# Kernel tuning notes

Hardware: AMD Instinct MI355X
Metric: run time of the kernel (lower is better)

The kernel has to match this reference:

```python
import jax, jax.numpy as jnp
from jax import lax
import numpy as np

DIM = 48
HEADS = 2
HIDDEN = 96  # int(dim * 2.0)
EPS_LN = 1e-5
EPS_NORM = 1e-12


def _ln(x, w, b):
    # WithBias LayerNorm over channel dim (dim=1 in NCHW == last dim in b,(hw),c)
    mu = jnp.mean(x, axis=1, keepdims=True)
    var = jnp.var(x, axis=1, keepdims=True)
    return (x - mu) / jnp.sqrt(var + EPS_LN) * w[None, :, None, None] + b[None, :, None, None]


def _conv1x1(x, w, b):
    # w: [O, C, 1, 1]
    return jnp.einsum('bchw,oc->bohw', x, w[:, :, 0, 0]) + b[None, :, None, None]


def _dwconv3(x, w, b):
    # w: [C, 1, 3, 3], groups=C
    y = lax.conv_general_dilated(x, w, (1, 1), 'SAME',
                                 feature_group_count=x.shape[1],
                                 dimension_numbers=('NCHW', 'OIHW', 'NCHW'))
    return y + b[None, :, None, None]


def _l2norm(x):
    n = jnp.sqrt(jnp.sum(x * x, axis=-1, keepdims=True))
    return x / jnp.maximum(n, EPS_NORM)


def setup_inputs() -> dict:
    key = jax.random.key(0)
    ks = jax.random.split(key, 12)
    s = 0.02
    inp = {
        'x': jax.random.normal(ks[0], (2, DIM, 64, 64), jnp.float32),
        'norm1_w': jnp.ones((DIM,), jnp.float32),
        'norm1_b': jnp.zeros((DIM,), jnp.float32),
        'qkv_w': jax.random.normal(ks[1], (DIM * 3, DIM, 1, 1), jnp.float32) * s,
        'qkv_b': jnp.zeros((DIM * 3,), jnp.float32),
        'qkvdw_w': jax.random.normal(ks[2], (DIM * 3, 1, 3, 3), jnp.float32) * s,
        'qkvdw_b': jnp.zeros((DIM * 3,), jnp.float32),
        'temperature': jnp.ones((HEADS, 1, 1), jnp.float32),
        'proj_w': jax.random.normal(ks[3], (DIM, DIM, 1, 1), jnp.float32) * s,
        'proj_b': jnp.zeros((DIM,), jnp.float32),
        'norm2_w': jnp.ones((DIM,), jnp.float32),
        'norm2_b': jnp.zeros((DIM,), jnp.float32),
        'fi_w': jax.random.normal(ks[4], (HIDDEN * 2, DIM, 1, 1), jnp.float32) * s,
        'fi_b': jnp.zeros((HIDDEN * 2,), jnp.float32),
        'fdw_w': jax.random.normal(ks[5], (HIDDEN * 2, 1, 3, 3), jnp.float32) * s,
        'fdw_b': jnp.zeros((HIDDEN * 2,), jnp.float32),
        'fo_w': jax.random.normal(ks[6], (DIM, HIDDEN, 1, 1), jnp.float32) * s,
        'fo_b': jnp.zeros((DIM,), jnp.float32),
    }
    return inp


def _block(x, norm1_w, norm1_b, qkv_w, qkv_b, qkvdw_w, qkvdw_b, temperature,
           proj_w, proj_b, norm2_w, norm2_b, fi_w, fi_b, fdw_w, fdw_b, fo_w, fo_b):
    b, c, h, w = x.shape
    n = h * w
    chead = c // HEADS
    # --- attention branch ---
    xn = _ln(x, norm1_w, norm1_b)
    qkv = _dwconv3(_conv1x1(xn, qkv_w, qkv_b), qkvdw_w, qkvdw_b)
    q, k, v = jnp.split(qkv, 3, axis=1)
    def to_heads(t):  # [b, heads*chead, h, w] -> [b, heads, n, chead]
        return t.reshape(b, HEADS, chead, n).transpose(0, 1, 3, 2)
    q, k, v = to_heads(q), to_heads(k), to_heads(v)
    q = _l2norm(q)
    k = _l2norm(k)
    attn = jnp.einsum('bhnc,bhmc->bhnm', q, k) * temperature[None]
    attn = jax.nn.softmax(attn, axis=-1)
    out = jnp.einsum('bhnm,bhmc->bhnc', attn, v)
    out = out.transpose(0, 1, 3, 2).reshape(b, c, h, w)
    x = x + _conv1x1(out, proj_w, proj_b)
    # --- ffn branch ---
    xn = _ln(x, norm2_w, norm2_b)
    y = _dwconv3(_conv1x1(xn, fi_w, fi_b), fdw_w, fdw_b)
    y1, y2 = jnp.split(y, 2, axis=1)
    y = jax.nn.gelu(y1, approximate=False) * y2
    x = x + _conv1x1(y, fo_w, fo_b)
    return x


def reference(x, norm1_w, norm1_b, qkv_w, qkv_b, qkvdw_w, qkvdw_b, temperature,
              proj_w, proj_b, norm2_w, norm2_b, fi_w, fi_b, fdw_w, fdw_b, fo_w, fo_b):
    return _block(x, norm1_w, norm1_b, qkv_w, qkv_b, qkvdw_w, qkvdw_b, temperature,
                  proj_w, proj_b, norm2_w, norm2_b, fi_w, fi_b, fdw_w, fdw_b, fo_w, fo_b)
```

## Files before the change

### kernel.cpp

```cpp
#include <hip/hip_runtime.h>
#include <hip/hip_bf16.h>
#include <math.h>

#define NPIX 4096
#define DIMC 48
#define NB 2
#define SPLIT 4

typedef __attribute__((ext_vector_type(8))) short short8;
typedef __attribute__((ext_vector_type(4))) short short4s;
typedef __attribute__((ext_vector_type(4))) float floatx4;

static __device__ inline short f2bf(float f) {
    union { float f; unsigned u; } v; v.f = f;
    unsigned r = (v.u + 0x7FFFu + ((v.u >> 16) & 1u)) >> 16;
    return (short)r;
}
static __device__ inline float bf2f(short s) {
    union { unsigned u; float f; } v;
    v.u = ((unsigned)(unsigned short)s) << 16;
    return v.f;
}
static __device__ inline unsigned pk2(float a, float b) {
    __hip_bfloat162 pk = __float22bfloat162_rn(make_float2(a, b));
    return *(unsigned*)&pk;
}

__global__ void k_prepw(const float* __restrict__ qkvw, const float* __restrict__ fiw,
                        const float* __restrict__ fow, const float* __restrict__ projw,
                        short* __restrict__ qkvwbf, short* __restrict__ fiwbf,
                        short* __restrict__ fowbf, short* __restrict__ projwbf) {
    int idx = blockIdx.x * 256 + threadIdx.x;
    if (idx < 144 * 64) {
        int o = idx >> 6, c = idx & 63;
        qkvwbf[idx] = (c < 48) ? f2bf(qkvw[o * 48 + c]) : (short)0;
        return;
    }
    idx -= 144 * 64;
    if (idx < 192 * 64) {
        int o = idx >> 6, c = idx & 63;
        fiwbf[idx] = (c < 48) ? f2bf(fiw[o * 48 + c]) : (short)0;
        return;
    }
    idx -= 192 * 64;
    if (idx < 48 * 96) {
        fowbf[idx] = f2bf(fow[idx]);
        return;
    }
    idx -= 48 * 96;
    if (idx < 48 * 64) {
        int o = idx >> 6, c = idx & 63;
        projwbf[idx] = (c < 48) ? f2bf(projw[o * 48 + c]) : (short)0;
    }
}

__global__ __launch_bounds__(256) void k_ln_conv_mfma(
    const float* __restrict__ xin, const float* __restrict__ lw, const float* __restrict__ lb,
    const short* __restrict__ wbf, const float* __restrict__ cb,
    short* __restrict__ outbf, int OC)
{
    int px0 = blockIdx.x * 32;
    int b = blockIdx.y;
    int t = threadIdx.x;
    int w = t >> 6, lane = t & 63, l15 = lane & 15, quad = lane >> 4;

    __shared__ float psum[8][32], psq[8][32];
    __shared__ float muS[32], rsS[32];
    __shared__ short xnbf[32][72];

    int px = t & 31, g = t >> 5;
    *(unsigned*)&xnbf[px][48 + g * 2] = 0u;

    float v[6];
    float s = 0.f, sq = 0.f;
#pragma unroll
    for (int i = 0; i < 6; i++) {
        v[i] = xin[((size_t)b * 48 + g * 6 + i) * (size_t)NPIX + px0 + px];
        s += v[i]; sq += v[i] * v[i];
    }
    psum[g][px] = s; psq[g][px] = sq;
    __syncthreads();
    if (t < 32) {
        float ss = 0.f, qq = 0.f;
#pragma unroll
        for (int i = 0; i < 8; i++) { ss += psum[i][t]; qq += psq[i][t]; }
        float mu = ss * (1.f / 48.f);
        float var = qq * (1.f / 48.f) - mu * mu;
        muS[t] = mu; rsS[t] = rsqrtf(var + 1e-5f);
    }
    __syncthreads();
    {
        float mu = muS[px], rs = rsS[px];
#pragma unroll
        for (int i = 0; i < 6; i++) {
            int c = g * 6 + i;
            xnbf[px][c] = f2bf((v[i] - mu) * rs * lw[c] + lb[c]);
        }
    }
    __syncthreads();
    floatx4 zf = {0.f, 0.f, 0.f, 0.f};
    int oct = OC >> 4;
    int njobs = 2 * oct;
    for (int job = w; job < njobs; job += 4) {
        int pt = job / oct, ot = job % oct;
        short8 a0 = *(const short8*)&xnbf[pt * 16 + l15][quad * 8];
        short8 a1 = *(const short8*)&xnbf[pt * 16 + l15][32 + quad * 8];
        const short* wb = wbf + (ot * 16 + l15) * 64;
        short8 b0 = *(const short8*)(wb + quad * 8);
        short8 b1 = *(const short8*)(wb + 32 + quad * 8);
        floatx4 c = __builtin_amdgcn_mfma_f32_16x16x32_bf16(a0, b0, zf, 0, 0, 0);
        c = __builtin_amdgcn_mfma_f32_16x16x32_bf16(a1, b1, c, 0, 0, 0);
        int oc = ot * 16 + l15;
        float bi = cb[oc];
        short4s st;
#pragma unroll
        for (int r = 0; r < 4; r++) st[r] = f2bf(c[r] + bi);
        *(short4s*)(outbf + ((size_t)b * OC + oc) * (size_t)NPIX + px0 + pt * 16 + quad * 4) = st;
    }
}

__global__ __launch_bounds__(256) void k_dw3heads(
    const short* __restrict__ qkv_pre, const float* __restrict__ dww,
    const float* __restrict__ dwb, const float* __restrict__ temp,
    short* __restrict__ Qbf, short* __restrict__ Kbf, short* __restrict__ Vbf)
{
    int px0 = blockIdx.x * 16;
    int y = blockIdx.y, b = blockIdx.z;
    int t = threadIdx.x;
    int wx0 = px0 - 8; if (wx0 < 0) wx0 = 0; if (wx0 > 32) wx0 = 32;
    int xoff = px0 - wx0;

    __shared__ short stage[3][144][40];
    __shared__ float q2[16][148];

    for (int seg = t; seg < 3 * 144 * 4; seg += 256) {
        int q = seg & 3, idx = seg >> 2;
        int c = idx % 144, r = idx / 144;
        int yy = y + r - 1;
        short8 ld = {};
        if ((unsigned)yy < 64u)
            ld = *(const short8*)(qkv_pre + (size_t)(b * 144 + c) * NPIX + yy * 64 + wx0 + q * 8);
        *(short8*)&stage[r][c][q * 8] = ld;
    }
    __syncthreads();
    int px = t & 15, g = t >> 4;
    {
        int sbase = xoff + px;
        for (int i = 0; i < 9; i++) {
            int c = g * 9 + i;
            const float* wp = dww + c * 9;
            float acc = dwb[c];
#pragma unroll
            for (int dy = 0; dy < 3; dy++) {
#pragma unroll
                for (int dx = -1; dx <= 1; dx++) {
                    int si = sbase + dx;
                    if ((unsigned)si < 32u)
                        acc += bf2f(stage[dy][c][si]) * wp[dy * 3 + dx + 1];
                }
            }
            q2[px][c] = acc;
        }
    }
    __syncthreads();
    if (t < 32) {
        int hpx = t & 15, h = t >> 4;
        int n = y * 64 + px0 + hpx;
        int bh = b * 2 + h;
        float q[24], k[24], vv[24]; float sqs = 0.f, sks = 0.f;
#pragma unroll
        for (int c = 0; c < 24; c++) {
            q[c] = q2[hpx][h * 24 + c];       sqs += q[c] * q[c];
            k[c] = q2[hpx][48 + h * 24 + c];  sks += k[c] * k[c];
            vv[c] = q2[hpx][96 + h * 24 + c];
        }
        float rq = temp[h] / fmaxf(sqrtf(sqs), 1e-12f);
        float rk = 1.f / fmaxf(sqrtf(sks), 1e-12f);
        short qs[32], ks[32];
#pragma unroll
        for (int c = 0; c < 24; c++) { qs[c] = f2bf(q[c] * rq); ks[c] = f2bf(k[c] * rk); }
#pragma unroll
        for (int c = 24; c < 32; c++) { qs[c] = 0; ks[c] = 0; }
        size_t ro = ((size_t)bh * NPIX + n) * 32;
#pragma unroll
        for (int i = 0; i < 4; i++) {
            short8 a, bb;
#pragma unroll
            for (int j = 0; j < 8; j++) { a[j] = qs[i * 8 + j]; bb[j] = ks[i * 8 + j]; }
            *(short8*)(Qbf + ro + i * 8) = a;
            *(short8*)(Kbf + ro + i * 8) = bb;
        }
        int r5 = n & 31;
        int pos = (r5 < 16) ? ((r5 >> 2) * 8 + (r5 & 3))
                            : (((r5 & 15) >> 2) * 8 + (r5 & 3) + 4);
        int vcol = (n & ~31) + pos;
#pragma unroll
        for (int c = 0; c < 24; c++)
            Vbf[((size_t)bh * 32 + c) * NPIX + vcol] = f2bf(vv[c]);
#pragma unroll
        for (int c = 24; c < 32; c++)
            Vbf[((size_t)bh * 32 + c) * NPIX + vcol] = 0;
    }
}

__global__ __launch_bounds__(256) void k_attn_mfma(const short* __restrict__ Qbf,
                                                   const short* __restrict__ Kbf,
                                                   const short* __restrict__ Vbf,
                                                   float* __restrict__ Opart,
                                                   float* __restrict__ lpart) {
    int qt = blockIdx.x, s = blockIdx.y, bh = blockIdx.z;
    int t = threadIdx.x;
    int w = t >> 6, lane = t & 63, l15 = lane & 15, quad = lane >> 4;

    __shared__ short tileK[2][64][40];
    __shared__ short tileV[2][32][72];

    int qrow0 = qt * 64 + w * 16;
    short8 bq = *(const short8*)(Qbf + ((size_t)bh * NPIX + qrow0 + l15) * 32 + quad * 8);

    int krow = t >> 2, kseg = t & 3;
    int vch = t >> 3, vseg = t & 7;
    const short* srcK = Kbf + ((size_t)bh * NPIX + krow) * 32 + kseg * 8;
    const short* srcV = Vbf + ((size_t)(bh * 32 + vch)) * NPIX + vseg * 8;

    int key0 = s * (NPIX / SPLIT);
    *(short8*)&tileK[0][krow][kseg * 8] = *(const short8*)(srcK + (size_t)key0 * 32);
    *(short8*)&tileV[0][vch][vseg * 8]  = *(const short8*)(srcV + key0);

    floatx4 zf = {0.f, 0.f, 0.f, 0.f};
    floatx4 o0 = zf, o1 = zf;
    float ls = 0.f;

    const int NKT = (NPIX / SPLIT) / 64;
    for (int kt = 0; kt < NKT; kt++) {
        __syncthreads();
        int cur = kt & 1;
        short8 ldK = {}, ldV = {};
        if (kt < NKT - 1) {
            int kabs = key0 + (kt + 1) * 64;
            ldK = *(const short8*)(srcK + (size_t)kabs * 32);
            ldV = *(const short8*)(srcV + kabs);
        }
        short8 ka0 = *(const short8*)&tileK[cur][l15][quad * 8];
        short8 ka1 = *(const short8*)&tileK[cur][16 + l15][quad * 8];
        short8 ka2 = *(const short8*)&tileK[cur][32 + l15][quad * 8];
        short8 ka3 = *(const short8*)&tileK[cur][48 + l15][quad * 8];
        floatx4 s0 = __builtin_amdgcn_mfma_f32_16x16x32_bf16(ka0, bq, zf, 0, 0, 0);
        floatx4 s1 = __builtin_amdgcn_mfma_f32_16x16x32_bf16(ka1, bq, zf, 0, 0, 0);
        floatx4 s2 = __builtin_amdgcn_mfma_f32_16x16x32_bf16(ka2, bq, zf, 0, 0, 0);
        floatx4 s3 = __builtin_amdgcn_mfma_f32_16x16x32_bf16(ka3, bq, zf, 0, 0, 0);
        float e0[4], e1[4], e2[4], e3[4];
#pragma unroll
        for (int r = 0; r < 4; r++) {
            e0[r] = __expf(s0[r]); e1[r] = __expf(s1[r]);
            e2[r] = __expf(s2[r]); e3[r] = __expf(s3[r]);
            ls += (e0[r] + e1[r]) + (e2[r] + e3[r]);
        }
        short8 p01, p23;
        {
            unsigned* u01 = (unsigned*)&p01;
            unsigned* u23 = (unsigned*)&p23;
            u01[0] = pk2(e0[0], e0[1]); u01[1] = pk2(e0[2], e0[3]);
            u01[2] = pk2(e1[0], e1[1]); u01[3] = pk2(e1[2], e1[3]);
            u23[0] = pk2(e2[0], e2[1]); u23[1] = pk2(e2[2], e2[3]);
            u23[2] = pk2(e3[0], e3[1]); u23[3] = pk2(e3[2], e3[3]);
        }
        short8 va00 = *(const short8*)&tileV[cur][l15][quad * 8];
        short8 va01 = *(const short8*)&tileV[cur][l15][32 + quad * 8];
        short8 va10 = *(const short8*)&tileV[cur][16 + l15][quad * 8];
        short8 va11 = *(const short8*)&tileV[cur][16 + l15][32 + quad * 8];
        o0 = __builtin_amdgcn_mfma_f32_16x16x32_bf16(va00, p01, o0, 0, 0, 0);
        o0 = __builtin_amdgcn_mfma_f32_16x16x32_bf16(va01, p23, o0, 0, 0, 0);
        o1 = __builtin_amdgcn_mfma_f32_16x16x32_bf16(va10, p01, o1, 0, 0, 0);
        o1 = __builtin_amdgcn_mfma_f32_16x16x32_bf16(va11, p23, o1, 0, 0, 0);
        if (kt < NKT - 1) {
            *(short8*)&tileK[1 - cur][krow][kseg * 8] = ldK;
            *(short8*)&tileV[1 - cur][vch][vseg * 8]  = ldV;
        }
    }
    ls += __shfl_xor(ls, 16, 64);
    ls += __shfl_xor(ls, 32, 64);
    int n = qrow0 + l15;
    size_t base2 = (size_t)(bh * SPLIT + s) * 32;
#pragma unroll
    for (int r = 0; r < 4; r++) {
        Opart[(base2 + quad * 4 + r) * NPIX + n] = o0[r];
        Opart[(base2 + 16 + quad * 4 + r) * NPIX + n] = o1[r];
    }
    if (quad == 0) lpart[((size_t)(bh * SPLIT + s)) * NPIX + n] = ls;
}

__global__ __launch_bounds__(256) void k_projlnfi(
    const float* __restrict__ x, const float* __restrict__ Opart,
    const float* __restrict__ lpart, const short* __restrict__ projwbf,
    const float* __restrict__ projb,
    const float* __restrict__ n2w, const float* __restrict__ n2b,
    const short* __restrict__ fiwbf, const float* __restrict__ fib,
    float* __restrict__ x1, short* __restrict__ fp_pre)
{
    int px0 = blockIdx.x * 32;
    int b = blockIdx.y;
    int t = threadIdx.x;
    int w = t >> 6, lane = t & 63, l15 = lane & 15, quad = lane >> 4;

    __shared__ __align__(16) short Ash[32][72];
    __shared__ float rlsh[2][32];
    __shared__ float x1sh[32][53];
    __shared__ float psum[8][32], psq[8][32];
    __shared__ float muS[32], rsS[32];
    __shared__ short xnbf[32][72];

    if (t < 64) {
        int h = t >> 5, px = t & 31;
        float l = 0.f;
#pragma unroll
        for (int s = 0; s < SPLIT; s++)
            l += lpart[((size_t)((b * 2 + h) * SPLIT + s)) * NPIX + px0 + px];
        rlsh[h][px] = 1.f / l;
    }
    {
        int px = t & 31, j = t >> 5;
        *(unsigned*)&Ash[px][48 + j * 2] = 0u;
        *(unsigned*)&xnbf[px][48 + j * 2] = 0u;
    }
    __syncthreads();
#pragma unroll
    for (int pi = 0; pi < 6; pi++) {
        int idx = pi * 256 + t;
        int px = idx & 31, c = idx >> 5;
        int h = c / 24, ch = c % 24;
        float acc = 0.f;
#pragma unroll
        for (int s = 0; s < SPLIT; s++)
            acc += Opart[(((size_t)((b * 2 + h) * SPLIT + s)) * 32 + ch) * NPIX + px0 + px];
        Ash[px][c] = f2bf(acc * rlsh[h][px]);
    }
    __syncthreads();
    floatx4 zf = {0.f, 0.f, 0.f, 0.f};
    for (int job = w; job < 6; job += 4) {
        int pt = job / 3, ot = job % 3;
        short8 a0 = *(const short8*)&Ash[pt * 16 + l15][quad * 8];
        short8 a1 = *(const short8*)&Ash[pt * 16 + l15][32 + quad * 8];
        const short* wb = projwbf + (ot * 16 + l15) * 64;
        short8 b0 = *(const short8*)(wb + quad * 8);
        short8 b1 = *(const short8*)(wb + 32 + quad * 8);
        floatx4 c = __builtin_amdgcn_mfma_f32_16x16x32_bf16(a0, b0, zf, 0, 0, 0);
        c = __builtin_amdgcn_mfma_f32_16x16x32_bf16(a1, b1, c, 0, 0, 0);
        int oc = ot * 16 + l15;
        float bi = projb[oc];
#pragma unroll
        for (int r = 0; r < 4; r++) {
            int px = pt * 16 + quad * 4 + r;
            size_t idx = ((size_t)b * 48 + oc) * NPIX + px0 + px;
            float val = x[idx] + c[r] + bi;
            x1[idx] = val;
            x1sh[px][oc] = val;
        }
    }
    __syncthreads();
    int px = t & 31, g = t >> 5;
    float v[6];
    float s = 0.f, sq = 0.f;
#pragma unroll
    for (int i = 0; i < 6; i++) {
        v[i] = x1sh[px][g * 6 + i];
        s += v[i]; sq += v[i] * v[i];
    }
    psum[g][px] = s; psq[g][px] = sq;
    __syncthreads();
    if (t < 32) {
        float ss = 0.f, qq = 0.f;
#pragma unroll
        for (int i = 0; i < 8; i++) { ss += psum[i][t]; qq += psq[i][t]; }
        float mu = ss * (1.f / 48.f);
        float var = qq * (1.f / 48.f) - mu * mu;
        muS[t] = mu; rsS[t] = rsqrtf(var + 1e-5f);
    }
    __syncthreads();
    {
        float mu = muS[px], rs = rsS[px];
#pragma unroll
        for (int i = 0; i < 6; i++) {
            int c = g * 6 + i;
            xnbf[px][c] = f2bf((v[i] - mu) * rs * n2w[c] + n2b[c]);
        }
    }
    __syncthreads();
    for (int job = w; job < 24; job += 4) {
        int pt = job / 12, ot = job % 12;
        short8 a0 = *(const short8*)&xnbf[pt * 16 + l15][quad * 8];
        short8 a1 = *(const short8*)&xnbf[pt * 16 + l15][32 + quad * 8];
        const short* wb = fiwbf + (ot * 16 + l15) * 64;
        short8 b0 = *(const short8*)(wb + quad * 8);
        short8 b1 = *(const short8*)(wb + 32 + quad * 8);
        floatx4 c = __builtin_amdgcn_mfma_f32_16x16x32_bf16(a0, b0, zf, 0, 0, 0);
        c = __builtin_amdgcn_mfma_f32_16x16x32_bf16(a1, b1, c, 0, 0, 0);
        int oc = ot * 16 + l15;
        float bi = fib[oc];
        short4s st;
#pragma unroll
        for (int r = 0; r < 4; r++) st[r] = f2bf(c[r] + bi);
        *(short4s*)(fp_pre + ((size_t)b * 192 + oc) * (size_t)NPIX + px0 + pt * 16 + quad * 4) = st;
    }
}

__global__ __launch_bounds__(256) void k_dwgatefo(
    const short* __restrict__ fp_pre, const float* __restrict__ fdww,
    const float* __restrict__ fdwb, const short* __restrict__ fowbf,
    const float* __restrict__ fob, const float* __restrict__ x1,
    float* __restrict__ out)
{
    int px0 = blockIdx.x * 16;
    int y = blockIdx.y, b = blockIdx.z;
    int t = threadIdx.x;
    int w = t >> 6, lane = t & 63, l15 = lane & 15, quad = lane >> 4;
    int wx0 = px0 - 8; if (wx0 < 0) wx0 = 0; if (wx0 > 32) wx0 = 32;
    int xoff = px0 - wx0;

    __shared__ short stage[3][192][40];
    __shared__ short yv[16][104];

    for (int seg = t; seg < 3 * 192 * 4; seg += 256) {
        int q = seg & 3, idx = seg >> 2;
        int c = idx % 192, r = idx / 192;
        int yy = y + r - 1;
        short8 ld = {};
        if ((unsigned)yy < 64u)
            ld = *(const short8*)(fp_pre + (size_t)(b * 192 + c) * NPIX + yy * 64 + wx0 + q * 8);
        *(short8*)&stage[r][c][q * 8] = ld;
    }
    __syncthreads();
    int px = t & 15, g = t >> 4;
    {
        int sbase = xoff + px;
        for (int i = 0; i < 6; i++) {
            int c = g * 6 + i;
            const float* wp  = fdww + c * 9;
            const float* wp2 = fdww + (c + 96) * 9;
            float a  = fdwb[c];
            float g2 = fdwb[c + 96];
#pragma unroll
            for (int dy = 0; dy < 3; dy++) {
#pragma unroll
                for (int dx = -1; dx <= 1; dx++) {
                    int si = sbase + dx;
                    if ((unsigned)si < 32u) {
                        a  += bf2f(stage[dy][c][si])      * wp[dy * 3 + dx + 1];
                        g2 += bf2f(stage[dy][c + 96][si]) * wp2[dy * 3 + dx + 1];
                    }
                }
            }
            float ge = 0.5f * a * (1.f + erff(a * 0.70710678118654752f));
            yv[px][c] = f2bf(ge * g2);
        }
    }
    __syncthreads();
    if (w < 3) {
        floatx4 c = {0.f, 0.f, 0.f, 0.f};
#pragma unroll
        for (int k = 0; k < 3; k++) {
            short8 a = *(const short8*)&yv[l15][k * 32 + quad * 8];
            short8 bb = *(const short8*)(fowbf + (w * 16 + l15) * 96 + k * 32 + quad * 8);
            c = __builtin_amdgcn_mfma_f32_16x16x32_bf16(a, bb, c, 0, 0, 0);
        }
        int oc = w * 16 + l15;
        float bi = fob[oc];
#pragma unroll
        for (int r = 0; r < 4; r++) {
            int n = y * 64 + px0 + quad * 4 + r;
            size_t idx = ((size_t)b * 48 + oc) * NPIX + n;
            out[idx] = x1[idx] + c[r] + bi;
        }
    }
}

extern "C" void kernel_launch(void* const* d_in, const int* in_sizes, int n_in,
                              void* d_out, int out_size, void* d_ws, size_t ws_size,
                              hipStream_t stream) {
    const float* x       = (const float*)d_in[0];
    const float* n1w     = (const float*)d_in[1];
    const float* n1b     = (const float*)d_in[2];
    const float* qkv_w   = (const float*)d_in[3];
    const float* qkv_b   = (const float*)d_in[4];
    const float* qkvdw_w = (const float*)d_in[5];
    const float* qkvdw_b = (const float*)d_in[6];
    const float* temp    = (const float*)d_in[7];
    const float* proj_w  = (const float*)d_in[8];
    const float* proj_b  = (const float*)d_in[9];
    const float* n2w     = (const float*)d_in[10];
    const float* n2b     = (const float*)d_in[11];
    const float* fi_w    = (const float*)d_in[12];
    const float* fi_b    = (const float*)d_in[13];
    const float* fdw_w   = (const float*)d_in[14];
    const float* fdw_b   = (const float*)d_in[15];
    const float* fo_w    = (const float*)d_in[16];
    const float* fo_b    = (const float*)d_in[17];

    float* ws = (float*)d_ws;
    short* qkv_pre = (short*)ws;
    short* fp_pre  = (short*)(ws + 589824);
    short* Qbf     = (short*)(ws + 1376256);
    short* Kbf     = (short*)(ws + 1638400);
    short* Vbf     = (short*)(ws + 1900544);
    float* Opart   = ws + 2162688;
    float* lpart   = ws + 4259840;
    float* x1      = ws + 4325376;
    short* qkvwbf  = (short*)(ws + 4718592);
    short* fiwbf   = qkvwbf + 9216;
    short* fowbf   = fiwbf + 12288;
    short* projwbf = fowbf + 4608;

    {
        int total = 144 * 64 + 192 * 64 + 48 * 96 + 48 * 64;
        k_prepw<<<(total + 255) / 256, 256, 0, stream>>>(qkv_w, fi_w, fo_w, proj_w,
                                                         qkvwbf, fiwbf, fowbf, projwbf);
    }
    {
        dim3 g(128, NB);
        k_ln_conv_mfma<<<g, 256, 0, stream>>>(x, n1w, n1b, qkvwbf, qkv_b, qkv_pre, 144);
    }
    {
        dim3 g(4, 64, NB);
        k_dw3heads<<<g, 256, 0, stream>>>(qkv_pre, qkvdw_w, qkvdw_b, temp, Qbf, Kbf, Vbf);
    }
    {
        dim3 g(64, SPLIT, 4);
        k_attn_mfma<<<g, 256, 0, stream>>>(Qbf, Kbf, Vbf, Opart, lpart);
    }
    {
        dim3 g(128, NB);
        k_projlnfi<<<g, 256, 0, stream>>>(x, Opart, lpart, projwbf, proj_b,
                                          n2w, n2b, fiwbf, fi_b, x1, fp_pre);
    }
    {
        dim3 g(4, 64, NB);
        k_dwgatefo<<<g, 256, 0, stream>>>(fp_pre, fdw_w, fdw_b, fowbf, fo_b, x1,
                                          (float*)d_out);
    }
}
```

Baseline: 149.6 us.

## Fuse pipeline into three kernels with halo recompute and in-block attention split-K combine

```diff
diff --git a/kernel.cpp b/kernel.cpp
--- a/kernel.cpp
+++ b/kernel.cpp
@@ -3,9 +3,7 @@
 #include <math.h>
 
 #define NPIX 4096
-#define DIMC 48
 #define NB 2
-#define SPLIT 4
 
 typedef __attribute__((ext_vector_type(8))) short short8;
 typedef __attribute__((ext_vector_type(4))) short short4s;
@@ -50,188 +48,182 @@
     idx -= 48 * 96;
     if (idx < 48 * 64) {
         int o = idx >> 6, c = idx & 63;
-        projwbf[idx] = (c < 48) ? f2bf(projw[o * 48 + c]) : (short)0;
-    }
-}
-
-__global__ __launch_bounds__(256) void k_ln_conv_mfma(
-    const float* __restrict__ xin, const float* __restrict__ lw, const float* __restrict__ lb,
-    const short* __restrict__ wbf, const float* __restrict__ cb,
-    short* __restrict__ outbf, int OC)
+        int h = c >> 5, cc = c & 31;
+        projwbf[idx] = (cc < 24) ? f2bf(projw[o * 48 + h * 24 + cc]) : (short)0;
+    }
+}
+
+__global__ __launch_bounds__(256) void k_qkv_fused(
+    const float* __restrict__ xin, const float* __restrict__ n1w, const float* __restrict__ n1b,
+    const short* __restrict__ qkvwbf, const float* __restrict__ qkvb,
+    const float* __restrict__ dww, const float* __restrict__ dwb,
+    const float* __restrict__ temp,
+    short* __restrict__ Qbf, short* __restrict__ Kbf, short* __restrict__ Vbf)
 {
-    int px0 = blockIdx.x * 32;
-    int b = blockIdx.y;
+    int px0 = blockIdx.x * 16;
+    int y = blockIdx.y, b = blockIdx.z;
     int t = threadIdx.x;
     int w = t >> 6, lane = t & 63, l15 = lane & 15, quad = lane >> 4;
 
-    __shared__ float psum[8][32], psq[8][32];
-    __shared__ float muS[32], rsS[32];
-    __shared__ short xnbf[32][72];
-
-    int px = t & 31, g = t >> 5;
-    *(unsigned*)&xnbf[px][48 + g * 2] = 0u;
-
-    float v[6];
-    float s = 0.f, sq = 0.f;
-#pragma unroll
-    for (int i = 0; i < 6; i++) {
-        v[i] = xin[((size_t)b * 48 + g * 6 + i) * (size_t)NPIX + px0 + px];
-        s += v[i]; sq += v[i] * v[i];
-    }
-    psum[g][px] = s; psq[g][px] = sq;
-    __syncthreads();
-    if (t < 32) {
-        float ss = 0.f, qq = 0.f;
-#pragma unroll
-        for (int i = 0; i < 8; i++) { ss += psum[i][t]; qq += psq[i][t]; }
+    __shared__ __align__(16) short xn[64][72];
+    __shared__ short qkv[64][148];
+    __shared__ float q2[16][148];
+    __shared__ float red[4][64], redq[4][64];
+    __shared__ float muS[64], rsS[64];
+    __shared__ float dwwS[1296], dwbS[144];
+    __shared__ short vmask[64];
+
+    for (int u = t; u < 1296; u += 256) dwwS[u] = dww[u];
+    if (t < 144) dwbS[t] = dwb[t];
+
+    int pp = t & 63, cg = t >> 6;
+    int rr = pp / 18, ix = pp - rr * 18;
+    int yy = y + rr - 1, xpx = px0 - 1 + ix;
+    bool pv = (pp < 54) && ((unsigned)yy < 64u) && ((unsigned)xpx < 64u);
+    if (cg == 0) vmask[pp] = pv ? (short)1 : (short)0;
+
+    float v[12]; float s = 0.f, sq = 0.f;
+    if (pv) {
+        size_t pbase = (size_t)(yy * 64 + xpx);
+#pragma unroll
+        for (int j = 0; j < 12; j++) {
+            float vv = xin[((size_t)b * 48 + cg * 12 + j) * NPIX + pbase];
+            v[j] = vv; s += vv; sq += vv * vv;
+        }
+    } else {
+#pragma unroll
+        for (int j = 0; j < 12; j++) v[j] = 0.f;
+    }
+    red[cg][pp] = s; redq[cg][pp] = sq;
+    __syncthreads();
+    if (t < 64) {
+        float ss = red[0][t] + red[1][t] + red[2][t] + red[3][t];
+        float qq = redq[0][t] + redq[1][t] + redq[2][t] + redq[3][t];
         float mu = ss * (1.f / 48.f);
         float var = qq * (1.f / 48.f) - mu * mu;
         muS[t] = mu; rsS[t] = rsqrtf(var + 1e-5f);
     }
     __syncthreads();
     {
-        float mu = muS[px], rs = rsS[px];
-#pragma unroll
-        for (int i = 0; i < 6; i++) {
-            int c = g * 6 + i;
-            xnbf[px][c] = f2bf((v[i] - mu) * rs * lw[c] + lb[c]);
-        }
+        float mu = muS[pp], rs = rsS[pp];
+#pragma unroll
+        for (int j = 0; j < 12; j++) {
+            int c = cg * 12 + j;
+            xn[pp][c] = f2bf((v[j] - mu) * rs * n1w[c] + n1b[c]);
+        }
+        short8 z8 = {};
+        if (cg == 0) *(short8*)&xn[pp][48] = z8;
+        else if (cg == 1) *(short8*)&xn[pp][56] = z8;
     }
     __syncthreads();
     floatx4 zf = {0.f, 0.f, 0.f, 0.f};
-    int oct = OC >> 4;
-    int njobs = 2 * oct;
-    for (int job = w; job < njobs; job += 4) {
-        int pt = job / oct, ot = job % oct;
-        short8 a0 = *(const short8*)&xnbf[pt * 16 + l15][quad * 8];
-        short8 a1 = *(const short8*)&xnbf[pt * 16 + l15][32 + quad * 8];
-        const short* wb = wbf + (ot * 16 + l15) * 64;
+    for (int job = w; job < 36; job += 4) {
+        int pt = job / 9, ot = job % 9;
+        short8 a0 = *(const short8*)&xn[pt * 16 + l15][quad * 8];
+        short8 a1 = *(const short8*)&xn[pt * 16 + l15][32 + quad * 8];
+        const short* wb = qkvwbf + (ot * 16 + l15) * 64;
         short8 b0 = *(const short8*)(wb + quad * 8);
         short8 b1 = *(const short8*)(wb + 32 + quad * 8);
         floatx4 c = __builtin_amdgcn_mfma_f32_16x16x32_bf16(a0, b0, zf, 0, 0, 0);
         c = __builtin_amdgcn_mfma_f32_16x16x32_bf16(a1, b1, c, 0, 0, 0);
         int oc = ot * 16 + l15;
-        float bi = cb[oc];
-        short4s st;
-#pragma unroll
-        for (int r = 0; r < 4; r++) st[r] = f2bf(c[r] + bi);
-        *(short4s*)(outbf + ((size_t)b * OC + oc) * (size_t)NPIX + px0 + pt * 16 + quad * 4) = st;
-    }
-}
-
-__global__ __launch_bounds__(256) void k_dw3heads(
-    const short* __restrict__ qkv_pre, const float* __restrict__ dww,
-    const float* __restrict__ dwb, const float* __restrict__ temp,
-    short* __restrict__ Qbf, short* __restrict__ Kbf, short* __restrict__ Vbf)
+        float bi = qkvb[oc];
+#pragma unroll
+        for (int r = 0; r < 4; r++) {
+            int opp = pt * 16 + quad * 4 + r;
+            qkv[opp][oc] = vmask[opp] ? f2bf(c[r] + bi) : (short)0;
+        }
+    }
+    __syncthreads();
+    {
+        int i = t & 15, g = t >> 4;
+        for (int cc = 0; cc < 9; cc++) {
+            int c = g * 9 + cc;
+            const float* wp = dwwS + c * 9;
+            float acc = dwbS[c];
+#pragma unroll
+            for (int dy = 0; dy < 3; dy++)
+#pragma unroll
+                for (int dx = 0; dx < 3; dx++)
+                    acc += bf2f(qkv[dy * 18 + i + dx][c]) * wp[dy * 3 + dx];
+            q2[i][c] = acc;
+        }
+    }
+    __syncthreads();
+    if (t < 128) {
+        int i = t & 15, h = (t >> 4) & 1, sel = t >> 5;
+        int n = y * 64 + px0 + i;
+        int bh = b * 2 + h;
+        if (sel < 2) {
+            float vv2[24]; float ss = 0.f;
+            int base = sel * 48 + h * 24;
+#pragma unroll
+            for (int c = 0; c < 24; c++) { vv2[c] = q2[i][base + c]; ss += vv2[c] * vv2[c]; }
+            float sc = ((sel == 0) ? temp[h] : 1.f) / fmaxf(sqrtf(ss), 1e-12f);
+            short qs[32];
+#pragma unroll
+            for (int c = 0; c < 24; c++) qs[c] = f2bf(vv2[c] * sc);
+#pragma unroll
+            for (int c = 24; c < 32; c++) qs[c] = 0;
+            short* dst = ((sel == 0) ? Qbf : Kbf) + ((size_t)bh * NPIX + n) * 32;
+#pragma unroll
+            for (int i8 = 0; i8 < 4; i8++) {
+                short8 st;
+#pragma unroll
+                for (int j = 0; j < 8; j++) st[j] = qs[i8 * 8 + j];
+                *(short8*)(dst + i8 * 8) = st;
+            }
+        } else {
+            int half = sel - 2;
+            int r5 = n & 31;
+            int pos = (r5 < 16) ? ((r5 >> 2) * 8 + (r5 & 3))
+                                : (((r5 & 15) >> 2) * 8 + (r5 & 3) + 4);
+            int vcol = (n & ~31) + pos;
+#pragma unroll
+            for (int cc = 0; cc < 12; cc++) {
+                int c = half * 12 + cc;
+                Vbf[((size_t)bh * 32 + c) * NPIX + vcol] = f2bf(q2[i][96 + h * 24 + c]);
+            }
+            if (half == 1) {
+#pragma unroll
+                for (int c = 24; c < 32; c++)
+                    Vbf[((size_t)bh * 32 + c) * NPIX + vcol] = 0;
+            }
+        }
+    }
+}
+
+__global__ __launch_bounds__(1024) void k_attn_mfma2(
+    const short* __restrict__ Qbf, const short* __restrict__ Kbf,
+    const short* __restrict__ Vbf, short* __restrict__ O)
 {
-    int px0 = blockIdx.x * 16;
-    int y = blockIdx.y, b = blockIdx.z;
+    int qt = blockIdx.x, bh = blockIdx.y;
     int t = threadIdx.x;
-    int wx0 = px0 - 8; if (wx0 < 0) wx0 = 0; if (wx0 > 32) wx0 = 32;
-    int xoff = px0 - wx0;
-
-    __shared__ short stage[3][144][40];
-    __shared__ float q2[16][148];
-
-    for (int seg = t; seg < 3 * 144 * 4; seg += 256) {
-        int q = seg & 3, idx = seg >> 2;
-        int c = idx % 144, r = idx / 144;
-        int yy = y + r - 1;
-        short8 ld = {};
-        if ((unsigned)yy < 64u)
-            ld = *(const short8*)(qkv_pre + (size_t)(b * 144 + c) * NPIX + yy * 64 + wx0 + q * 8);
-        *(short8*)&stage[r][c][q * 8] = ld;
-    }
-    __syncthreads();
-    int px = t & 15, g = t >> 4;
-    {
-        int sbase = xoff + px;
-        for (int i = 0; i < 9; i++) {
-            int c = g * 9 + i;
-            const float* wp = dww + c * 9;
-            float acc = dwb[c];
-#pragma unroll
-            for (int dy = 0; dy < 3; dy++) {
-#pragma unroll
-                for (int dx = -1; dx <= 1; dx++) {
-                    int si = sbase + dx;
-                    if ((unsigned)si < 32u)
-                        acc += bf2f(stage[dy][c][si]) * wp[dy * 3 + dx + 1];
-                }
-            }
-            q2[px][c] = acc;
-        }
-    }
-    __syncthreads();
-    if (t < 32) {
-        int hpx = t & 15, h = t >> 4;
-        int n = y * 64 + px0 + hpx;
-        int bh = b * 2 + h;
-        float q[24], k[24], vv[24]; float sqs = 0.f, sks = 0.f;
-#pragma unroll
-        for (int c = 0; c < 24; c++) {
-            q[c] = q2[hpx][h * 24 + c];       sqs += q[c] * q[c];
-            k[c] = q2[hpx][48 + h * 24 + c];  sks += k[c] * k[c];
-            vv[c] = q2[hpx][96 + h * 24 + c];
-        }
-        float rq = temp[h] / fmaxf(sqrtf(sqs), 1e-12f);
-        float rk = 1.f / fmaxf(sqrtf(sks), 1e-12f);
-        short qs[32], ks[32];
-#pragma unroll
-        for (int c = 0; c < 24; c++) { qs[c] = f2bf(q[c] * rq); ks[c] = f2bf(k[c] * rk); }
-#pragma unroll
-        for (int c = 24; c < 32; c++) { qs[c] = 0; ks[c] = 0; }
-        size_t ro = ((size_t)bh * NPIX + n) * 32;
-#pragma unroll
-        for (int i = 0; i < 4; i++) {
-            short8 a, bb;
-#pragma unroll
-            for (int j = 0; j < 8; j++) { a[j] = qs[i * 8 + j]; bb[j] = ks[i * 8 + j]; }
-            *(short8*)(Qbf + ro + i * 8) = a;
-            *(short8*)(Kbf + ro + i * 8) = bb;
-        }
-        int r5 = n & 31;
-        int pos = (r5 < 16) ? ((r5 >> 2) * 8 + (r5 & 3))
-                            : (((r5 & 15) >> 2) * 8 + (r5 & 3) + 4);
-        int vcol = (n & ~31) + pos;
-#pragma unroll
-        for (int c = 0; c < 24; c++)
-            Vbf[((size_t)bh * 32 + c) * NPIX + vcol] = f2bf(vv[c]);
-#pragma unroll
-        for (int c = 24; c < 32; c++)
-            Vbf[((size_t)bh * 32 + c) * NPIX + vcol] = 0;
-    }
-}
-
-__global__ __launch_bounds__(256) void k_attn_mfma(const short* __restrict__ Qbf,
-                                                   const short* __restrict__ Kbf,
-                                                   const short* __restrict__ Vbf,
-                                                   float* __restrict__ Opart,
-                                                   float* __restrict__ lpart) {
-    int qt = blockIdx.x, s = blockIdx.y, bh = blockIdx.z;
-    int t = threadIdx.x;
-    int w = t >> 6, lane = t & 63, l15 = lane & 15, quad = lane >> 4;
-
-    __shared__ short tileK[2][64][40];
-    __shared__ short tileV[2][32][72];
-
-    int qrow0 = qt * 64 + w * 16;
+    int tg = t & 255, g = t >> 8;
+    int wloc = (t >> 6) & 3, lane = t & 63, l15 = lane & 15, quad = lane >> 4;
+
+    __shared__ __align__(16) short tileK[4][2][64][40];
+    __shared__ __align__(16) short tileV[4][2][32][72];
+    __shared__ float Ocomb[4][64][33];
+    __shared__ float Lcomb[4][64];
+
+    int qrow0 = qt * 64 + wloc * 16;
     short8 bq = *(const short8*)(Qbf + ((size_t)bh * NPIX + qrow0 + l15) * 32 + quad * 8);
 
-    int krow = t >> 2, kseg = t & 3;
-    int vch = t >> 3, vseg = t & 7;
+    int krow = tg >> 2, kseg = tg & 3;
+    int vch = tg >> 3, vseg = tg & 7;
     const short* srcK = Kbf + ((size_t)bh * NPIX + krow) * 32 + kseg * 8;
     const short* srcV = Vbf + ((size_t)(bh * 32 + vch)) * NPIX + vseg * 8;
 
-    int key0 = s * (NPIX / SPLIT);
-    *(short8*)&tileK[0][krow][kseg * 8] = *(const short8*)(srcK + (size_t)key0 * 32);
-    *(short8*)&tileV[0][vch][vseg * 8]  = *(const short8*)(srcV + key0);
+    int key0 = g * 1024;
+    *(short8*)&tileK[g][0][krow][kseg * 8] = *(const short8*)(srcK + (size_t)key0 * 32);
+    *(short8*)&tileV[g][0][vch][vseg * 8]  = *(const short8*)(srcV + key0);
 
     floatx4 zf = {0.f, 0.f, 0.f, 0.f};
     floatx4 o0 = zf, o1 = zf;
     float ls = 0.f;
 
-    const int NKT = (NPIX / SPLIT) / 64;
+    const int NKT = 16;
     for (int kt = 0; kt < NKT; kt++) {
         __syncthreads();
         int cur = kt & 1;
@@ -241,10 +233,10 @@
             ldK = *(const short8*)(srcK + (size_t)kabs * 32);
             ldV = *(const short8*)(srcV + kabs);
         }
-        short8 ka0 = *(const short8*)&tileK[cur][l15][quad * 8];
-        short8 ka1 = *(const short8*)&tileK[cur][16 + l15][quad * 8];
-        short8 ka2 = *(const short8*)&tileK[cur][32 + l15][quad * 8];
-        short8 ka3 = *(const short8*)&tileK[cur][48 + l15][quad * 8];
+        short8 ka0 = *(const short8*)&tileK[g][cur][l15][quad * 8];
+        short8 ka1 = *(const short8*)&tileK[g][cur][16 + l15][quad * 8];
+        short8 ka2 = *(const short8*)&tileK[g][cur][32 + l15][quad * 8];
+        short8 ka3 = *(const short8*)&tileK[g][cur][48 + l15][quad * 8];
         floatx4 s0 = __builtin_amdgcn_mfma_f32_16x16x32_bf16(ka0, bq, zf, 0, 0, 0);
         floatx4 s1 = __builtin_amdgcn_mfma_f32_16x16x32_bf16(ka1, bq, zf, 0, 0, 0);
         floatx4 s2 = __builtin_amdgcn_mfma_f32_16x16x32_bf16(ka2, bq, zf, 0, 0, 0);
@@ -265,82 +257,86 @@
             u23[0] = pk2(e2[0], e2[1]); u23[1] = pk2(e2[2], e2[3]);
             u23[2] = pk2(e3[0], e3[1]); u23[3] = pk2(e3[2], e3[3]);
         }
-        short8 va00 = *(const short8*)&tileV[cur][l15][quad * 8];
-        short8 va01 = *(const short8*)&tileV[cur][l15][32 + quad * 8];
-        short8 va10 = *(const short8*)&tileV[cur][16 + l15][quad * 8];
-        short8 va11 = *(const short8*)&tileV[cur][16 + l15][32 + quad * 8];
+        short8 va00 = *(const short8*)&tileV[g][cur][l15][quad * 8];
+        short8 va01 = *(const short8*)&tileV[g][cur][l15][32 + quad * 8];
+        short8 va10 = *(const short8*)&tileV[g][cur][16 + l15][quad * 8];
+        short8 va11 = *(const short8*)&tileV[g][cur][16 + l15][32 + quad * 8];
         o0 = __builtin_amdgcn_mfma_f32_16x16x32_bf16(va00, p01, o0, 0, 0, 0);
         o0 = __builtin_amdgcn_mfma_f32_16x16x32_bf16(va01, p23, o0, 0, 0, 0);
         o1 = __builtin_amdgcn_mfma_f32_16x16x32_bf16(va10, p01, o1, 0, 0, 0);
         o1 = __builtin_amdgcn_mfma_f32_16x16x32_bf16(va11, p23, o1, 0, 0, 0);
         if (kt < NKT - 1) {
-            *(short8*)&tileK[1 - cur][krow][kseg * 8] = ldK;
-            *(short8*)&tileV[1 - cur][vch][vseg * 8]  = ldV;
+            *(short8*)&tileK[g][1 - cur][krow][kseg * 8] = ldK;
+            *(short8*)&tileV[g][1 - cur][vch][vseg * 8]  = ldV;
         }
     }
     ls += __shfl_xor(ls, 16, 64);
     ls += __shfl_xor(ls, 32, 64);
-    int n = qrow0 + l15;
-    size_t base2 = (size_t)(bh * SPLIT + s) * 32;
+    int qi = wloc * 16 + l15;
 #pragma unroll
     for (int r = 0; r < 4; r++) {
-        Opart[(base2 + quad * 4 + r) * NPIX + n] = o0[r];
-        Opart[(base2 + 16 + quad * 4 + r) * NPIX + n] = o1[r];
-    }
-    if (quad == 0) lpart[((size_t)(bh * SPLIT + s)) * NPIX + n] = ls;
-}
-
-__global__ __launch_bounds__(256) void k_projlnfi(
-    const float* __restrict__ x, const float* __restrict__ Opart,
-    const float* __restrict__ lpart, const short* __restrict__ projwbf,
-    const float* __restrict__ projb,
+        Ocomb[g][qi][quad * 4 + r]      = o0[r];
+        Ocomb[g][qi][16 + quad * 4 + r] = o1[r];
+    }
+    if (quad == 0) Lcomb[g][qi] = ls;
+    __syncthreads();
+    {
+        int qq = t >> 4, cp = t & 15;
+        float l4 = Lcomb[0][qq] + Lcomb[1][qq] + Lcomb[2][qq] + Lcomb[3][qq];
+        float inv = 1.f / l4;
+        float sa = (Ocomb[0][qq][2 * cp] + Ocomb[1][qq][2 * cp] +
+                    Ocomb[2][qq][2 * cp] + Ocomb[3][qq][2 * cp]) * inv;
+        float sb = (Ocomb[0][qq][2 * cp + 1] + Ocomb[1][qq][2 * cp + 1] +
+                    Ocomb[2][qq][2 * cp + 1] + Ocomb[3][qq][2 * cp + 1]) * inv;
+        int b = bh >> 1, h = bh & 1;
+        int n = qt * 64 + qq;
+        *(unsigned*)(O + ((size_t)b * NPIX + n) * 64 + h * 32 + 2 * cp) = pk2(sa, sb);
+    }
+}
+
+__global__ __launch_bounds__(256) void k_tail_fused(
+    const float* __restrict__ xin, const short* __restrict__ O,
+    const short* __restrict__ projwbf, const float* __restrict__ projb,
     const float* __restrict__ n2w, const float* __restrict__ n2b,
     const short* __restrict__ fiwbf, const float* __restrict__ fib,
-    float* __restrict__ x1, short* __restrict__ fp_pre)
+    const float* __restrict__ fdww, const float* __restrict__ fdwb,
+    const short* __restrict__ fowbf, const float* __restrict__ fob,
+    float* __restrict__ out)
 {
-    int px0 = blockIdx.x * 32;
-    int b = blockIdx.y;
+    int px0 = blockIdx.x * 16;
+    int y = blockIdx.y, b = blockIdx.z;
     int t = threadIdx.x;
     int w = t >> 6, lane = t & 63, l15 = lane & 15, quad = lane >> 4;
 
-    __shared__ __align__(16) short Ash[32][72];
-    __shared__ float rlsh[2][32];
-    __shared__ float x1sh[32][53];
-    __shared__ float psum[8][32], psq[8][32];
-    __shared__ float muS[32], rsS[32];
-    __shared__ short xnbf[32][72];
-
+    __shared__ float x1s[64][53];
+    __shared__ __align__(16) short xn2[64][72];
+    __shared__ short ypre[56][196];
+    __shared__ __align__(16) short yv[16][104];
+    __shared__ float red[4][64], redq[4][64];
+    __shared__ float muS[64], rsS[64];
+    __shared__ float fdwwS[1728], fdwbS[192];
+    __shared__ short vmask[64];
+    __shared__ int nidx[64];
+
+    for (int u = t; u < 1728; u += 256) fdwwS[u] = fdww[u];
+    if (t < 192) fdwbS[t] = fdwb[t];
     if (t < 64) {
-        int h = t >> 5, px = t & 31;
-        float l = 0.f;
-#pragma unroll
-        for (int s = 0; s < SPLIT; s++)
-            l += lpart[((size_t)((b * 2 + h) * SPLIT + s)) * NPIX + px0 + px];
-        rlsh[h][px] = 1.f / l;
-    }
-    {
-        int px = t & 31, j = t >> 5;
-        *(unsigned*)&Ash[px][48 + j * 2] = 0u;
-        *(unsigned*)&xnbf[px][48 + j * 2] = 0u;
-    }
-    __syncthreads();
-#pragma unroll
-    for (int pi = 0; pi < 6; pi++) {
-        int idx = pi * 256 + t;
-        int px = idx & 31, c = idx >> 5;
-        int h = c / 24, ch = c % 24;
-        float acc = 0.f;
-#pragma unroll
-        for (int s = 0; s < SPLIT; s++)
-            acc += Opart[(((size_t)((b * 2 + h) * SPLIT + s)) * 32 + ch) * NPIX + px0 + px];
-        Ash[px][c] = f2bf(acc * rlsh[h][px]);
-    }
-    __syncthreads();
+        int rr = t / 18, ix = t - rr * 18;
+        int yy = y + rr - 1, xpx = px0 - 1 + ix;
+        bool pv = (t < 54) && ((unsigned)yy < 64u) && ((unsigned)xpx < 64u);
+        vmask[t] = pv ? (short)1 : (short)0;
+        int n = yy * 64 + xpx;
+        n = n < 0 ? 0 : (n > 4095 ? 4095 : n);
+        nidx[t] = n;
+    }
+    __syncthreads();
+
     floatx4 zf = {0.f, 0.f, 0.f, 0.f};
-    for (int job = w; job < 6; job += 4) {
+    for (int job = w; job < 12; job += 4) {
         int pt = job / 3, ot = job % 3;
-        short8 a0 = *(const short8*)&Ash[pt * 16 + l15][quad * 8];
-        short8 a1 = *(const short8*)&Ash[pt * 16 + l15][32 + quad * 8];
+        const short* oa = O + ((size_t)b * NPIX + nidx[pt * 16 + l15]) * 64;
+        short8 a0 = *(const short8*)(oa + quad * 8);
+        short8 a1 = *(const short8*)(oa + 32 + quad * 8);
         const short* wb = projwbf + (ot * 16 + l15) * 64;
         short8 b0 = *(const short8*)(wb + quad * 8);
         short8 b1 = *(const short8*)(wb + 32 + quad * 8);
@@ -350,46 +346,44 @@
         float bi = projb[oc];
 #pragma unroll
         for (int r = 0; r < 4; r++) {
-            int px = pt * 16 + quad * 4 + r;
-            size_t idx = ((size_t)b * 48 + oc) * NPIX + px0 + px;
-            float val = x[idx] + c[r] + bi;
-            x1[idx] = val;
-            x1sh[px][oc] = val;
-        }
-    }
-    __syncthreads();
-    int px = t & 31, g = t >> 5;
-    float v[6];
-    float s = 0.f, sq = 0.f;
-#pragma unroll
-    for (int i = 0; i < 6; i++) {
-        v[i] = x1sh[px][g * 6 + i];
-        s += v[i]; sq += v[i] * v[i];
-    }
-    psum[g][px] = s; psq[g][px] = sq;
-    __syncthreads();
-    if (t < 32) {
-        float ss = 0.f, qq = 0.f;
-#pragma unroll
-        for (int i = 0; i < 8; i++) { ss += psum[i][t]; qq += psq[i][t]; }
-        float mu = ss * (1.f / 48.f);
-        float var = qq * (1.f / 48.f) - mu * mu;
-        muS[t] = mu; rsS[t] = rsqrtf(var + 1e-5f);
-    }
-    __syncthreads();
-    {
-        float mu = muS[px], rs = rsS[px];
-#pragma unroll
-        for (int i = 0; i < 6; i++) {
-            int c = g * 6 + i;
-            xnbf[px][c] = f2bf((v[i] - mu) * rs * n2w[c] + n2b[c]);
-        }
-    }
-    __syncthreads();
-    for (int job = w; job < 24; job += 4) {
+            int opp = pt * 16 + quad * 4 + r;
+            x1s[opp][oc] = xin[((size_t)b * 48 + oc) * NPIX + nidx[opp]] + c[r] + bi;
+        }
+    }
+    __syncthreads();
+    int pp = t & 63, cg = t >> 6;
+    {
+        float v[12]; float s = 0.f, sq = 0.f;
+#pragma unroll
+        for (int j = 0; j < 12; j++) {
+            float vv = x1s[pp][cg * 12 + j];
+            v[j] = vv; s += vv; sq += vv * vv;
+        }
+        red[cg][pp] = s; redq[cg][pp] = sq;
+        __syncthreads();
+        if (t < 64) {
+            float ss = red[0][t] + red[1][t] + red[2][t] + red[3][t];
+            float qq = redq[0][t] + redq[1][t] + redq[2][t] + redq[3][t];
+            float mu = ss * (1.f / 48.f);
+            float var = qq * (1.f / 48.f) - mu * mu;
+            muS[t] = mu; rsS[t] = rsqrtf(var + 1e-5f);
+        }
+        __syncthreads();
+        float mu = muS[pp], rs = rsS[pp];
+#pragma unroll
+        for (int j = 0; j < 12; j++) {
+            int c = cg * 12 + j;
+            xn2[pp][c] = f2bf((v[j] - mu) * rs * n2w[c] + n2b[c]);
+        }
+        short8 z8 = {};
+        if (cg == 0) *(short8*)&xn2[pp][48] = z8;
+        else if (cg == 1) *(short8*)&xn2[pp][56] = z8;
+    }
+    __syncthreads();
+    for (int job = w; job < 48; job += 4) {
         int pt = job / 12, ot = job % 12;
-        short8 a0 = *(const short8*)&xnbf[pt * 16 + l15][quad * 8];
-        short8 a1 = *(const short8*)&xnbf[pt * 16 + l15][32 + quad * 8];
+        short8 a0 = *(const short8*)&xn2[pt * 16 + l15][quad * 8];
+        short8 a1 = *(const short8*)&xn2[pt * 16 + l15][32 + quad * 8];
         const short* wb = fiwbf + (ot * 16 + l15) * 64;
         short8 b0 = *(const short8*)(wb + quad * 8);
         short8 b1 = *(const short8*)(wb + 32 + quad * 8);
@@ -397,69 +391,40 @@
         c = __builtin_amdgcn_mfma_f32_16x16x32_bf16(a1, b1, c, 0, 0, 0);
         int oc = ot * 16 + l15;
         float bi = fib[oc];
-        short4s st;
-#pragma unroll
-        for (int r = 0; r < 4; r++) st[r] = f2bf(c[r] + bi);
-        *(short4s*)(fp_pre + ((size_t)b * 192 + oc) * (size_t)NPIX + px0 + pt * 16 + quad * 4) = st;
-    }
-}
-
-__global__ __launch_bounds__(256) void k_dwgatefo(
-    const short* __restrict__ fp_pre, const float* __restrict__ fdww,
-    const float* __restrict__ fdwb, const short* __restrict__ fowbf,
-    const float* __restrict__ fob, const float* __restrict__ x1,
-    float* __restrict__ out)
-{
-    int px0 = blockIdx.x * 16;
-    int y = blockIdx.y, b = blockIdx.z;
-    int t = threadIdx.x;
-    int w = t >> 6, lane = t & 63, l15 = lane & 15, quad = lane >> 4;
-    int wx0 = px0 - 8; if (wx0 < 0) wx0 = 0; if (wx0 > 32) wx0 = 32;
-    int xoff = px0 - wx0;
-
-    __shared__ short stage[3][192][40];
-    __shared__ short yv[16][104];
-
-    for (int seg = t; seg < 3 * 192 * 4; seg += 256) {
-        int q = seg & 3, idx = seg >> 2;
-        int c = idx % 192, r = idx / 192;
-        int yy = y + r - 1;
-        short8 ld = {};
-        if ((unsigned)yy < 64u)
-            ld = *(const short8*)(fp_pre + (size_t)(b * 192 + c) * NPIX + yy * 64 + wx0 + q * 8);
-        *(short8*)&stage[r][c][q * 8] = ld;
-    }
-    __syncthreads();
-    int px = t & 15, g = t >> 4;
-    {
-        int sbase = xoff + px;
-        for (int i = 0; i < 6; i++) {
-            int c = g * 6 + i;
-            const float* wp  = fdww + c * 9;
-            const float* wp2 = fdww + (c + 96) * 9;
-            float a  = fdwb[c];
-            float g2 = fdwb[c + 96];
-#pragma unroll
-            for (int dy = 0; dy < 3; dy++) {
-#pragma unroll
-                for (int dx = -1; dx <= 1; dx++) {
-                    int si = sbase + dx;
-                    if ((unsigned)si < 32u) {
-                        a  += bf2f(stage[dy][c][si])      * wp[dy * 3 + dx + 1];
-                        g2 += bf2f(stage[dy][c + 96][si]) * wp2[dy * 3 + dx + 1];
-                    }
+#pragma unroll
+        for (int r = 0; r < 4; r++) {
+            int opp = pt * 16 + quad * 4 + r;
+            if (opp < 56) ypre[opp][oc] = vmask[opp] ? f2bf(c[r] + bi) : (short)0;
+        }
+    }
+    __syncthreads();
+    {
+        int i = t & 15, gg = t >> 4;
+        for (int cc = 0; cc < 6; cc++) {
+            int c = gg * 6 + cc;
+            const float* wp  = fdwwS + c * 9;
+            const float* wp2 = fdwwS + (c + 96) * 9;
+            float a = fdwbS[c], g2v = fdwbS[c + 96];
+#pragma unroll
+            for (int dy = 0; dy < 3; dy++)
+#pragma unroll
+                for (int dx = 0; dx < 3; dx++) {
+                    int ppi = dy * 18 + i + dx;
+                    a   += bf2f(ypre[ppi][c])      * wp[dy * 3 + dx];
+                    g2v += bf2f(ypre[ppi][c + 96]) * wp2[dy * 3 + dx];
                 }
-            }
             float ge = 0.5f * a * (1.f + erff(a * 0.70710678118654752f));
-            yv[px][c] = f2bf(ge * g2);
-        }
+            yv[i][c] = f2bf(ge * g2v);
+        }
+        short8 z8 = {};
+        if (gg == 0) *(short8*)&yv[i][96] = z8;
     }
     __syncthreads();
     if (w < 3) {
-        floatx4 c = {0.f, 0.f, 0.f, 0.f};
+        floatx4 c = zf;
 #pragma unroll
         for (int k = 0; k < 3; k++) {
-            short8 a = *(const short8*)&yv[l15][k * 32 + quad * 8];
+            short8 a  = *(const short8*)&yv[l15][k * 32 + quad * 8];
             short8 bb = *(const short8*)(fowbf + (w * 16 + l15) * 96 + k * 32 + quad * 8);
             c = __builtin_amdgcn_mfma_f32_16x16x32_bf16(a, bb, c, 0, 0, 0);
         }
@@ -467,9 +432,9 @@
         float bi = fob[oc];
 #pragma unroll
         for (int r = 0; r < 4; r++) {
-            int n = y * 64 + px0 + quad * 4 + r;
-            size_t idx = ((size_t)b * 48 + oc) * NPIX + n;
-            out[idx] = x1[idx] + c[r] + bi;
+            int i = quad * 4 + r;
+            size_t idx = ((size_t)b * 48 + oc) * NPIX + y * 64 + px0 + i;
+            out[idx] = x1s[19 + i][oc] + c[r] + bi;
         }
     }
 }
@@ -496,16 +461,12 @@
     const float* fo_w    = (const float*)d_in[16];
     const float* fo_b    = (const float*)d_in[17];
 
-    float* ws = (float*)d_ws;
-    short* qkv_pre = (short*)ws;
-    short* fp_pre  = (short*)(ws + 589824);
-    short* Qbf     = (short*)(ws + 1376256);
-    short* Kbf     = (short*)(ws + 1638400);
-    short* Vbf     = (short*)(ws + 1900544);
-    float* Opart   = ws + 2162688;
-    float* lpart   = ws + 4259840;
-    float* x1      = ws + 4325376;
-    short* qkvwbf  = (short*)(ws + 4718592);
+    short* sws = (short*)d_ws;
+    short* Qbf     = sws;
+    short* Kbf     = Qbf + 524288;
+    short* Vbf     = Kbf + 524288;
+    short* Obuf    = Vbf + 524288;
+    short* qkvwbf  = Obuf + 524288;
     short* fiwbf   = qkvwbf + 9216;
     short* fowbf   = fiwbf + 12288;
     short* projwbf = fowbf + 4608;
@@ -516,25 +477,18 @@
                                                          qkvwbf, fiwbf, fowbf, projwbf);
     }
     {
-        dim3 g(128, NB);
-        k_ln_conv_mfma<<<g, 256, 0, stream>>>(x, n1w, n1b, qkvwbf, qkv_b, qkv_pre, 144);
-    }
-    {
         dim3 g(4, 64, NB);
-        k_dw3heads<<<g, 256, 0, stream>>>(qkv_pre, qkvdw_w, qkvdw_b, temp, Qbf, Kbf, Vbf);
-    }
-    {
-        dim3 g(64, SPLIT, 4);
-        k_attn_mfma<<<g, 256, 0, stream>>>(Qbf, Kbf, Vbf, Opart, lpart);
-    }
-    {
-        dim3 g(128, NB);
-        k_projlnfi<<<g, 256, 0, stream>>>(x, Opart, lpart, projwbf, proj_b,
-                                          n2w, n2b, fiwbf, fi_b, x1, fp_pre);
+        k_qkv_fused<<<g, 256, 0, stream>>>(x, n1w, n1b, qkvwbf, qkv_b,
+                                           qkvdw_w, qkvdw_b, temp, Qbf, Kbf, Vbf);
+    }
+    {
+        dim3 g(64, 4);
+        k_attn_mfma2<<<g, 1024, 0, stream>>>(Qbf, Kbf, Vbf, Obuf);
     }
     {
         dim3 g(4, 64, NB);
-        k_dwgatefo<<<g, 256, 0, stream>>>(fp_pre, fdw_w, fdw_b, fowbf, fo_b, x1,
-                                          (float*)d_out);
-    }
-}
+        k_tail_fused<<<g, 256, 0, stream>>>(x, Obuf, projwbf, proj_b, n2w, n2b,
+                                            fiwbf, fi_b, fdw_w, fdw_b, fowbf, fo_b,
+                                            (float*)d_out);
+    }
+}
```

Measured after the change: 139.5 us. 6.8% less time.
